# Kernel optimization log

Measured on AMD Instinct MI355X. Metric: run time of the kernel, lower is better.

## Reference

```python
import jax, jax.numpy as jnp
import numpy as np

N_ELEM = 10   # len(EnvPara.ELEMENTS)
N_ATOMS = 100000
N_DIM = 256


def setup_inputs() -> dict:
    key = jax.random.key(0)
    k = jax.random.split(key, 5)
    return {
        "input_tensor": jax.random.normal(k[0], (N_ATOMS, N_DIM), jnp.float32),
        "species": jax.random.randint(k[1], (N_ATOMS,), 0, N_ELEM, dtype=jnp.int64),
        "W1": jax.random.normal(k[2], (N_ELEM, N_DIM, N_DIM), jnp.float32) / np.sqrt(N_DIM).astype(np.float32),
        "b1": jnp.zeros((N_ELEM, N_DIM), jnp.float32),
        "W2": jax.random.normal(k[3], (N_ELEM, N_DIM, 1), jnp.float32) / np.sqrt(N_DIM).astype(np.float32),
        "b2": jnp.zeros((N_ELEM, 1), jnp.float32),
    }


def _element_linear(x, species, W, b):
    # Species-routed linear: each atom uses the weight/bias of its element.
    # Loop over the small fixed element set (N_ELEM=10) to avoid materializing
    # a [n_atoms, d_in, d_out] gathered-weight tensor.
    out = jnp.zeros((x.shape[0], W.shape[2]), dtype=x.dtype)
    for e in range(W.shape[0]):
        mask = (species == e)[:, None]                      # [n_atoms, 1]
        out = out + jnp.where(mask, x @ W[e] + b[e], jnp.zeros((), x.dtype))
    return out


def reference(input_tensor, species, W1, b1, W2, b2):
    # layer2(silu(layer1(x)))
    h = _element_linear(input_tensor, species, W1, b1)      # [n_atoms, n_dim]
    h = jax.nn.silu(h)                                      # way=0 -> plain SiLU
    return _element_linear(h, species, W2, b2)              # [n_atoms, 1]
```

## Files before the change

### kernel.cpp

```cpp
#include <hip/hip_runtime.h>
#include <hip/hip_bf16.h>
#include <stdint.h>


#define NDIM 256
#define CHUNKS 16
#define BCHUNK 16384
#define TROWS 32
#define ROWB 1040
#define MAXT 16

typedef __attribute__((ext_vector_type(8))) short short8;
typedef __attribute__((ext_vector_type(8))) unsigned short ushort8;
typedef __attribute__((ext_vector_type(4))) float f32x4;

__device__ __forceinline__ unsigned short f2bf(float f) {
  unsigned u = __float_as_uint(f);
  u = (u + 0x7FFFu + ((u >> 16) & 1u)) >> 16;
  return (unsigned short)u;
}

__device__ __forceinline__ void gload_lds16(const void* gsrc, void* ldst) {
  __builtin_amdgcn_global_load_lds(
      (const __attribute__((address_space(1))) unsigned*)gsrc,
      (__attribute__((address_space(3))) unsigned*)(uintptr_t)(unsigned)(uintptr_t)ldst,
      16, 0, 0);
}

__device__ __forceinline__ short8 cvt8(float4 lo, float4 hi) {
  union { short8 s; unsigned u[4]; } r;
  __hip_bfloat162 t;
  t = __float22bfloat162_rn(make_float2(lo.x, lo.y)); r.u[0] = *(unsigned*)&t;
  t = __float22bfloat162_rn(make_float2(lo.z, lo.w)); r.u[1] = *(unsigned*)&t;
  t = __float22bfloat162_rn(make_float2(hi.x, hi.y)); r.u[2] = *(unsigned*)&t;
  t = __float22bfloat162_rn(make_float2(hi.z, hi.w)); r.u[3] = *(unsigned*)&t;
  return r.s;
}


__global__ void convw_k(const float* __restrict__ W1, unsigned short* __restrict__ wt, int NE) {
  int t = blockIdx.x * 256 + threadIdx.x;
  if (t >= NE * 8192) return;
  int n = t & 255;
  int g = (t >> 8) & 3;
  int step = (t >> 10) & 7;
  int e = t >> 13;
  int k0 = step * 32 + g * 8;
  const float* src = W1 + ((size_t)e << 16) + (size_t)k0 * NDIM + n;
  unsigned short v[8];
  #pragma unroll
  for (int j = 0; j < 8; ++j) v[j] = f2bf(src[j * NDIM]);
  char* chunk = (char*)wt + (size_t)(e * 8 + step) * BCHUNK;
  unsigned off = ((unsigned)(n * 64 + g * 16)) ^ ((unsigned)((n & 7) << 4));
  *(ushort8*)(chunk + off) = *(ushort8*)v;
}

__global__ void bhist_k(const int* __restrict__ sp, int n, int* __restrict__ bc, int NE) {
  __shared__ int wc[4][16];
  int tid = threadIdx.x;
  int i = blockIdx.x * 256 + tid;
  int s = (i < n) ? sp[i] : -1;
  int w = tid >> 6, lane = tid & 63;
  for (int e = 0; e < NE; ++e) {
    unsigned long long m = __ballot(s == e);
    if (lane == 0) wc[w][e] = __popcll(m);
  }
  __syncthreads();
  if (tid < NE) bc[blockIdx.x * NE + tid] = wc[0][tid] + wc[1][tid] + wc[2][tid] + wc[3][tid];
}

__global__ void scan_k(const int* __restrict__ bc, int* __restrict__ bo,
                       int* __restrict__ atom_start, int* __restrict__ tile_off,
                       int nblocks, int NE) {
  __shared__ int csum[256];
  __shared__ int coff[256];
  __shared__ int stot[16];
  __shared__ int sbase[16];
  int tid = threadIdx.x;
  int per = (nblocks + CHUNKS - 1) / CHUNKS;
  int e = tid / CHUNKS, c = tid % CHUNKS;
  int b0 = c * per, b1 = b0 + per; if (b1 > nblocks) b1 = nblocks;
  if (tid < NE * CHUNKS) {
    int s = 0;
    for (int b = b0; b < b1; ++b) s += bc[b * NE + e];
    csum[tid] = s;
  }
  __syncthreads();
  if (tid < NE) {
    int r = 0;
    for (int c2 = 0; c2 < CHUNKS; ++c2) { coff[tid * CHUNKS + c2] = r; r += csum[tid * CHUNKS + c2]; }
    stot[tid] = r;
  }
  __syncthreads();
  if (tid == 0) {
    int a = 0, t = 0;
    for (int e2 = 0; e2 < NE; ++e2) {
      sbase[e2] = a;
      atom_start[e2] = a; tile_off[e2] = t;
      a += stot[e2]; t += (stot[e2] + TROWS - 1) / TROWS;
    }
    atom_start[NE] = a; tile_off[NE] = t;
  }
  __syncthreads();
  if (tid < NE * CHUNKS) {
    int run = sbase[e] + coff[tid];
    for (int b = b0; b < b1; ++b) { bo[b * NE + e] = run; run += bc[b * NE + e]; }
  }
}

__global__ void dscatter_k(const int* __restrict__ sp, int n, const int* __restrict__ bo,
                           int* __restrict__ sorted, int NE) {
  __shared__ int wc[4][16];
  int tid = threadIdx.x;
  int i = blockIdx.x * 256 + tid;
  int s = (i < n) ? sp[i] : -1;
  int w = tid >> 6, lane = tid & 63;
  for (int e = 0; e < NE; ++e) {
    unsigned long long m = __ballot(s == e);
    if (lane == 0) wc[w][e] = __popcll(m);
  }
  __syncthreads();
  for (int e = 0; e < NE; ++e) {
    unsigned long long m = __ballot(s == e);
    if (s == e) {
      int wpre = 0;
      for (int w2 = 0; w2 < 4; ++w2) if (w2 < w) wpre += wc[w2][e];
      int rank = __popcll(m & ((1ull << lane) - 1ull));
      sorted[bo[blockIdx.x * NE + e] + wpre + rank] = i;
    }
  }
}


__global__ __launch_bounds__(512, 2) void gemm_k(
    const float* __restrict__ x, const unsigned short* __restrict__ wt,
    const float* __restrict__ b1, const float* __restrict__ w2,
    const float* __restrict__ b2, const int* __restrict__ sorted,
    const int* __restrict__ atom_start, const int* __restrict__ tile_off,
    float* __restrict__ out, int NE)
{
  __shared__ __align__(16) char ldsA[3][TROWS * ROWB];
  __shared__ float partLds[256];
  __shared__ int ldsAtoms[MAXT * TROWS];
  __shared__ int toffs[17], astart[17];

  int tid = threadIdx.x, lane = tid & 63, wid = tid >> 6;
  int lr = lane & 15, lg = lane >> 4;

  if (tid <= NE) { toffs[tid] = tile_off[tid]; astart[tid] = atom_start[tid]; }
  __syncthreads();

  int ntiles = toffs[NE];
  int nb = gridDim.x, b = blockIdx.x;
  int q = ntiles / nb, rem = ntiles % nb;
  int t0 = b * q + (b < rem ? b : rem);
  int cnt = q + (b < rem ? 1 : 0);
  if (cnt <= 0) return;
  if (cnt > MAXT) cnt = MAXT;
  int t1 = t0 + cnt;

  for (int i = tid; i < cnt * TROWS; i += 512) {
    int tt = t0 + i / TROWS, r = i % TROWS;
    int e = 0;
    while (tt >= toffs[e + 1]) ++e;
    int rs = astart[e] + (tt - toffs[e]) * TROWS;
    int rv = astart[e + 1] - rs; if (rv > TROWS) rv = TROWS;
    ldsAtoms[i] = sorted[rs + (r < rv ? r : rv - 1)];
  }
  __syncthreads();

  auto stageA = [&](int t, int buf) {
    int base = (t - t0) * TROWS;
    #pragma unroll
    for (int i = 0; i < 4; ++i) {
      int rrow = wid * 4 + i;
      int atom = ldsAtoms[base + rrow];
      gload_lds16(x + (size_t)atom * NDIM + lane * 4, &ldsA[buf][rrow * ROWB]);
    }
  };

  int held_e = -1;
  short8 bf[2][8];
  float bbv[2], wvv[2], b2v = 0.f;

  stageA(t0, 0);
  stageA(t0 + 1 < t1 ? t0 + 1 : t1 - 1, 1);

  for (int t = t0; t < t1; ++t) {
    int buf = (t - t0) % 3;
    int e = 0;
    while (t >= toffs[e + 1]) ++e;

    int ts = t + 2 < t1 ? t + 2 : t1 - 1;
    stageA(ts, (t - t0 + 2) % 3);

    if (e != held_e) {
      held_e = e;
      const char* wbase = (const char*)wt + (size_t)e * 8 * BCHUNK;
      #pragma unroll
      for (int nf = 0; nf < 2; ++nf) {
        int ncol = wid * 32 + nf * 16 + lr;
        unsigned off = ((unsigned)(ncol * 64 + lg * 16)) ^ ((unsigned)((ncol & 7) << 4));
        #pragma unroll
        for (int s = 0; s < 8; ++s)
          bf[nf][s] = *(const short8*)(wbase + (size_t)s * BCHUNK + off);
        bbv[nf] = b1[(size_t)e * NDIM + ncol];
        wvv[nf] = w2[(size_t)e * NDIM + ncol];
      }
      b2v = b2[e];
    }

    if (t == t0)            { asm volatile("s_waitcnt vmcnt(8)" ::: "memory"); }
    else if (t == t0 + 1)   { asm volatile("s_waitcnt vmcnt(9)" ::: "memory"); }
    else                    { asm volatile("s_waitcnt vmcnt(10)" ::: "memory"); }
    __builtin_amdgcn_s_barrier();
    __builtin_amdgcn_sched_barrier(0);

    f32x4 acc[2][2];
    const f32x4 zero = {0.f, 0.f, 0.f, 0.f};
    #pragma unroll
    for (int i = 0; i < 2; ++i)
      #pragma unroll
      for (int j = 0; j < 2; ++j) acc[i][j] = zero;

    const char* Ab = ldsA[buf];
    #pragma unroll
    for (int step = 0; step < 8; ++step) {
      int k0 = step * 32;
      short8 af[2];
      #pragma unroll
      for (int mf = 0; mf < 2; ++mf) {
        const char* p = Ab + (mf * 16 + lr) * ROWB + (k0 + lg * 8) * 4;
        float4 lo = *(const float4*)p;
        float4 hi = *(const float4*)(p + 16);
        af[mf] = cvt8(lo, hi);
      }
      #pragma unroll
      for (int mf = 0; mf < 2; ++mf)
        #pragma unroll
        for (int nf = 0; nf < 2; ++nf)
          acc[mf][nf] = __builtin_amdgcn_mfma_f32_16x16x32_bf16(af[mf], bf[nf][step], acc[mf][nf], 0, 0, 0);
    }

    float psum[2][4];
    #pragma unroll
    for (int mf = 0; mf < 2; ++mf)
      #pragma unroll
      for (int rg = 0; rg < 4; ++rg) psum[mf][rg] = 0.f;

    #pragma unroll
    for (int nf = 0; nf < 2; ++nf) {
      #pragma unroll
      for (int mf = 0; mf < 2; ++mf)
        #pragma unroll
        for (int rg = 0; rg < 4; ++rg) {
          float h = acc[mf][nf][rg] + bbv[nf];
          float sv = h * __builtin_amdgcn_rcpf(1.f + __expf(-h));
          psum[mf][rg] += sv * wvv[nf];
        }
    }
    #pragma unroll
    for (int mf = 0; mf < 2; ++mf)
      #pragma unroll
      for (int rg = 0; rg < 4; ++rg) {
        float v = psum[mf][rg];
        v += __shfl_xor(v, 1, 64);
        v += __shfl_xor(v, 2, 64);
        v += __shfl_xor(v, 4, 64);
        v += __shfl_xor(v, 8, 64);
        psum[mf][rg] = v;
      }
    if (lr == 0) {
      #pragma unroll
      for (int mf = 0; mf < 2; ++mf)
        #pragma unroll
        for (int rg = 0; rg < 4; ++rg)
          partLds[wid * TROWS + mf * 16 + lg * 4 + rg] = psum[mf][rg];
    }

    asm volatile("s_waitcnt lgkmcnt(0)" ::: "memory");
    __builtin_amdgcn_s_barrier();
    __builtin_amdgcn_sched_barrier(0);

    if (tid < TROWS) {
      float s = b2v;
      #pragma unroll
      for (int w = 0; w < 8; ++w) s += partLds[w * TROWS + tid];
      out[ldsAtoms[(t - t0) * TROWS + tid]] = s;
    }
  }
}


extern "C" void kernel_launch(void* const* d_in, const int* in_sizes, int n_in,
                              void* d_out, int out_size, void* d_ws, size_t ws_size,
                              hipStream_t stream) {
  const float* x  = (const float*)d_in[0];
  const int*   sp = (const int*)d_in[1];
  const float* W1 = (const float*)d_in[2];
  const float* b1 = (const float*)d_in[3];
  const float* W2 = (const float*)d_in[4];
  const float* b2 = (const float*)d_in[5];
  float* out = (float*)d_out;

  int n_atoms = in_sizes[0] / NDIM;
  int NE = in_sizes[2] / (NDIM * NDIM);
  int nblocks = (n_atoms + 255) / 256;

  char* wsb = (char*)d_ws;
  size_t o = 0;
  int* bc = (int*)(wsb + o);         o += ((size_t)nblocks * NE * 4 + 255) & ~(size_t)255;
  int* bo = (int*)(wsb + o);         o += ((size_t)nblocks * NE * 4 + 255) & ~(size_t)255;
  int* atom_start = (int*)(wsb + o); o += 256;
  int* tile_off   = (int*)(wsb + o); o += 256;
  int* sorted     = (int*)(wsb + o); o += ((size_t)n_atoms * 4 + 255) & ~(size_t)255;
  unsigned short* wt = (unsigned short*)(wsb + o);

  hipLaunchKernelGGL(convw_k, dim3((NE * 8192 + 255) / 256), dim3(256), 0, stream,
                     W1, wt, NE);
  hipLaunchKernelGGL(bhist_k, dim3(nblocks), dim3(256), 0, stream, sp, n_atoms, bc, NE);
  hipLaunchKernelGGL(scan_k, dim3(1), dim3(256), 0, stream, bc, bo, atom_start, tile_off,
                     nblocks, NE);
  hipLaunchKernelGGL(dscatter_k, dim3(nblocks), dim3(256), 0, stream, sp, n_atoms, bo,
                     sorted, NE);

  hipLaunchKernelGGL(gemm_k, dim3(256), dim3(512), 0, stream,
                     x, wt, b1, W2, b2, sorted, atom_start, tile_off, out, NE);
}
```

Measured before the change: 74.79 us.

## Partition GEMM blocks per element so each block holds one weight set

The scan kernel now hands out the fixed count of GEMM blocks to elements in proportion to each element's tile count, and writes per-element block start offsets. Each GEMM block then works on tiles of a single element, so it loads its bf16 weight fragments, biases and W2 column once up front, instead of checking and reloading them whenever a tile crosses an element boundary. The atom-index gather is simplified to one contiguous range, and the final per-row reduction is spread across all waves. Launch bounds are relaxed to one block per CU. The MAXT clamp is removed, so uneven allocation could overflow the LDS atom buffer if a block gets more than 16 tiles.

```diff
diff --git a/kernel.cpp b/kernel.cpp
--- a/kernel.cpp
+++ b/kernel.cpp
@@ -9,6 +9,7 @@
 #define TROWS 32
 #define ROWB 1040
 #define MAXT 16
+#define NB_GEMM 256
 
 typedef __attribute__((ext_vector_type(8))) short short8;
 typedef __attribute__((ext_vector_type(8))) unsigned short ushort8;
@@ -71,7 +72,7 @@
 
 __global__ void scan_k(const int* __restrict__ bc, int* __restrict__ bo,
                        int* __restrict__ atom_start, int* __restrict__ tile_off,
-                       int nblocks, int NE) {
+                       int* __restrict__ bstart, int nblocks, int NE) {
   __shared__ int csum[256];
   __shared__ int coff[256];
   __shared__ int stot[16];
@@ -100,6 +101,19 @@
       a += stot[e2]; t += (stot[e2] + TROWS - 1) / TROWS;
     }
     atom_start[NE] = a; tile_off[NE] = t;
+    int ntl = t > 0 ? t : 1;
+    int nbk[16]; int tot = 0, emax = 0;
+    for (int e2 = 0; e2 < NE; ++e2) {
+      int nt = tile_off[e2 + 1] - tile_off[e2];
+      int v = (nt > 0) ? (int)(((long long)nt * NB_GEMM) / ntl) : 0;
+      if (nt > 0 && v < 1) v = 1;
+      nbk[e2] = v; tot += v;
+      if (nbk[e2] > nbk[emax]) emax = e2;
+    }
+    nbk[emax] += NB_GEMM - tot;
+    int bacc = 0;
+    for (int e2 = 0; e2 < NE; ++e2) { bstart[e2] = bacc; bacc += nbk[e2]; }
+    bstart[NE] = bacc;
   }
   __syncthreads();
   if (tid < NE * CHUNKS) {
@@ -132,42 +146,68 @@
 }
 
 
-__global__ __launch_bounds__(512, 2) void gemm_k(
+__global__ __launch_bounds__(512, 1) void gemm_k(
     const float* __restrict__ x, const unsigned short* __restrict__ wt,
     const float* __restrict__ b1, const float* __restrict__ w2,
     const float* __restrict__ b2, const int* __restrict__ sorted,
     const int* __restrict__ atom_start, const int* __restrict__ tile_off,
-    float* __restrict__ out, int NE)
+    const int* __restrict__ bstart, float* __restrict__ out, int NE)
 {
   __shared__ __align__(16) char ldsA[3][TROWS * ROWB];
   __shared__ float partLds[256];
   __shared__ int ldsAtoms[MAXT * TROWS];
-  __shared__ int toffs[17], astart[17];
+  __shared__ int toffs[17], astart[17], bst[17];
 
   int tid = threadIdx.x, lane = tid & 63, wid = tid >> 6;
   int lr = lane & 15, lg = lane >> 4;
 
-  if (tid <= NE) { toffs[tid] = tile_off[tid]; astart[tid] = atom_start[tid]; }
-  __syncthreads();
-
-  int ntiles = toffs[NE];
-  int nb = gridDim.x, b = blockIdx.x;
-  int q = ntiles / nb, rem = ntiles % nb;
-  int t0 = b * q + (b < rem ? b : rem);
-  int cnt = q + (b < rem ? 1 : 0);
+  if (tid <= NE) {
+    toffs[tid] = tile_off[tid]; astart[tid] = atom_start[tid]; bst[tid] = bstart[tid];
+  }
+  __syncthreads();
+
+  int b = blockIdx.x;
+  int e = 0;
+  while (b >= bst[e + 1]) ++e;
+  int j = b - bst[e], nbe = bst[e + 1] - bst[e];
+  int nte = toffs[e + 1] - toffs[e];
+  int q = nte / nbe, r = nte % nbe;
+  int cnt = q + (j < r ? 1 : 0);
   if (cnt <= 0) return;
-  if (cnt > MAXT) cnt = MAXT;
+  int t0 = toffs[e] + j * q + (j < r ? j : r);
   int t1 = t0 + cnt;
 
-  for (int i = tid; i < cnt * TROWS; i += 512) {
-    int tt = t0 + i / TROWS, r = i % TROWS;
-    int e = 0;
-    while (tt >= toffs[e + 1]) ++e;
-    int rs = astart[e] + (tt - toffs[e]) * TROWS;
-    int rv = astart[e + 1] - rs; if (rv > TROWS) rv = TROWS;
-    ldsAtoms[i] = sorted[rs + (r < rv ? r : rv - 1)];
-  }
-  __syncthreads();
+  {
+    int rs0 = astart[e] + (t0 - toffs[e]) * TROWS;
+    int rvAll = astart[e + 1] - rs0;
+    for (int i = tid; i < cnt * TROWS; i += 512) {
+      int rloc = (i < rvAll) ? i : (rvAll - 1);
+      ldsAtoms[i] = sorted[rs0 + rloc];
+    }
+  }
+  __syncthreads();
+
+  short8 bf[2][8];
+  float bbv[2], wvv[2];
+  {
+    const char* wbase = (const char*)wt + (size_t)e * 8 * BCHUNK;
+    #pragma unroll
+    for (int nf = 0; nf < 2; ++nf) {
+      int ncol = wid * 32 + nf * 16 + lr;
+      unsigned off = ((unsigned)(ncol * 64 + lg * 16)) ^ ((unsigned)((ncol & 7) << 4));
+      #pragma unroll
+      for (int s = 0; s < 8; ++s)
+        bf[nf][s] = *(const short8*)(wbase + (size_t)s * BCHUNK + off);
+      bbv[nf] = b1[(size_t)e * NDIM + ncol];
+      wvv[nf] = w2[(size_t)e * NDIM + ncol];
+    }
+  }
+  float b2v = b2[e];
+  #pragma unroll
+  for (int nf = 0; nf < 2; ++nf)
+    #pragma unroll
+    for (int s = 0; s < 8; ++s)
+      asm volatile("" :: "v"(bf[nf][s]));
 
   auto stageA = [&](int t, int buf) {
     int base = (t - t0) * TROWS;
@@ -179,40 +219,18 @@
     }
   };
 
-  int held_e = -1;
-  short8 bf[2][8];
-  float bbv[2], wvv[2], b2v = 0.f;
-
   stageA(t0, 0);
   stageA(t0 + 1 < t1 ? t0 + 1 : t1 - 1, 1);
 
   for (int t = t0; t < t1; ++t) {
     int buf = (t - t0) % 3;
-    int e = 0;
-    while (t >= toffs[e + 1]) ++e;
 
     int ts = t + 2 < t1 ? t + 2 : t1 - 1;
     stageA(ts, (t - t0 + 2) % 3);
 
-    if (e != held_e) {
-      held_e = e;
-      const char* wbase = (const char*)wt + (size_t)e * 8 * BCHUNK;
-      #pragma unroll
-      for (int nf = 0; nf < 2; ++nf) {
-        int ncol = wid * 32 + nf * 16 + lr;
-        unsigned off = ((unsigned)(ncol * 64 + lg * 16)) ^ ((unsigned)((ncol & 7) << 4));
-        #pragma unroll
-        for (int s = 0; s < 8; ++s)
-          bf[nf][s] = *(const short8*)(wbase + (size_t)s * BCHUNK + off);
-        bbv[nf] = b1[(size_t)e * NDIM + ncol];
-        wvv[nf] = w2[(size_t)e * NDIM + ncol];
-      }
-      b2v = b2[e];
-    }
-
-    if (t == t0)            { asm volatile("s_waitcnt vmcnt(8)" ::: "memory"); }
-    else if (t == t0 + 1)   { asm volatile("s_waitcnt vmcnt(9)" ::: "memory"); }
-    else                    { asm volatile("s_waitcnt vmcnt(10)" ::: "memory"); }
+    if (t == t0)          { asm volatile("s_waitcnt vmcnt(8)" ::: "memory"); }
+    else if (t == t0 + 1) { asm volatile("s_waitcnt vmcnt(9)" ::: "memory"); }
+    else                  { asm volatile("s_waitcnt vmcnt(10)" ::: "memory"); }
     __builtin_amdgcn_s_barrier();
     __builtin_amdgcn_sched_barrier(0);
 
@@ -221,7 +239,7 @@
     #pragma unroll
     for (int i = 0; i < 2; ++i)
       #pragma unroll
-      for (int j = 0; j < 2; ++j) acc[i][j] = zero;
+      for (int jj = 0; jj < 2; ++jj) acc[i][jj] = zero;
 
     const char* Ab = ldsA[buf];
     #pragma unroll
@@ -282,11 +300,12 @@
     __builtin_amdgcn_s_barrier();
     __builtin_amdgcn_sched_barrier(0);
 
-    if (tid < TROWS) {
+    if (lane < 4) {
+      int rloc = wid * 4 + lane;
       float s = b2v;
       #pragma unroll
-      for (int w = 0; w < 8; ++w) s += partLds[w * TROWS + tid];
-      out[ldsAtoms[(t - t0) * TROWS + tid]] = s;
+      for (int w = 0; w < 8; ++w) s += partLds[w * TROWS + rloc];
+      out[ldsAtoms[(t - t0) * TROWS + rloc]] = s;
     }
   }
 }
@@ -313,6 +332,7 @@
   int* bo = (int*)(wsb + o);         o += ((size_t)nblocks * NE * 4 + 255) & ~(size_t)255;
   int* atom_start = (int*)(wsb + o); o += 256;
   int* tile_off   = (int*)(wsb + o); o += 256;
+  int* bstart     = (int*)(wsb + o); o += 256;
   int* sorted     = (int*)(wsb + o); o += ((size_t)n_atoms * 4 + 255) & ~(size_t)255;
   unsigned short* wt = (unsigned short*)(wsb + o);
 
@@ -320,10 +340,10 @@
                      W1, wt, NE);
   hipLaunchKernelGGL(bhist_k, dim3(nblocks), dim3(256), 0, stream, sp, n_atoms, bc, NE);
   hipLaunchKernelGGL(scan_k, dim3(1), dim3(256), 0, stream, bc, bo, atom_start, tile_off,
-                     nblocks, NE);
+                     bstart, nblocks, NE);
   hipLaunchKernelGGL(dscatter_k, dim3(nblocks), dim3(256), 0, stream, sp, n_atoms, bo,
                      sorted, NE);
 
-  hipLaunchKernelGGL(gemm_k, dim3(256), dim3(512), 0, stream,
-                     x, wt, b1, W2, b2, sorted, atom_start, tile_off, out, NE);
-}
+  hipLaunchKernelGGL(gemm_k, dim3(NB_GEMM), dim3(512), 0, stream,
+                     x, wt, b1, W2, b2, sorted, atom_start, tile_off, bstart, out, NE);
+}
```

After: 75.90 us. No clear change (+1.5%).
